# Performance work log

Hardware: AMD Instinct MI355X
Metric: run time of the kernel (lower is better)

The kernel has to match this reference:

```python
import jax, jax.numpy as jnp
import numpy as np

INPUT_SIZE = 128
HIDDEN_SIZE = 1024
OMEGA_IN = 0.5
OMEGA_B = 0.1
RHO = 0.9
L, N = 2048, 32


def setup_inputs() -> dict:
    key = jax.random.key(0)
    k_in, k_b, k_h, k_x = jax.random.split(key, 4)
    x = jax.random.normal(k_x, (L, N, INPUT_SIZE), dtype=jnp.float32)
    h_init = jnp.zeros((N, HIDDEN_SIZE), dtype=jnp.float32)
    W_in = jax.random.uniform(k_in, (HIDDEN_SIZE, INPUT_SIZE), minval=-OMEGA_IN, maxval=OMEGA_IN, dtype=jnp.float32)
    bias = jax.random.uniform(k_b, (HIDDEN_SIZE,), minval=-OMEGA_B, maxval=OMEGA_B, dtype=jnp.float32)
    # recurrent matrix rescaled to spectral radius RHO (as in the torch __init__)
    W_h_np = np.asarray(jax.random.uniform(k_h, (HIDDEN_SIZE, HIDDEN_SIZE), minval=-1.0, maxval=1.0, dtype=jnp.float32))
    sr = np.abs(np.linalg.eigvals(W_h_np)).max()
    W_h = jnp.asarray((W_h_np / sr * RHO).astype(np.float32))
    return {"input": x, "h_init": h_init, "W_in": W_in, "bias": bias, "W_h": W_h}


def reference(input, h_init, W_in, bias, W_h):
    # Pre-compute input projection for all timesteps in one GEMM: (L,N,H)
    x_proj = jnp.einsum('lni,hi->lnh', input, W_in) + bias

    def step(h, xp_t):
        h = jnp.tanh(xp_t + h @ W_h.T)
        return h, h

    _, states = jax.lax.scan(step, h_init, x_proj)
    return states  # (L, N, H)
```

## Files before the change

### kernel.cpp

```cpp
#include <hip/hip_runtime.h>
#include <stdint.h>

#define LSTEPS 2048
#define NB 32
#define IS 128
#define HS 1024
#define NGROUPS 8
#define WPG 32
#define BPG 4
#define CPW 32
#define NTHREADS 256
#define FLAG_SLOTS 8


__global__ __launch_bounds__(NTHREADS, 1)
void reservoir_scan(const float* __restrict__ x,
                    const float* __restrict__ h_init,
                    const float* __restrict__ W_in,
                    const float* __restrict__ bias,
                    const float* __restrict__ W_h,
                    float* __restrict__ out,
                    unsigned int* __restrict__ flags) {
  const int b    = blockIdx.x;
  const int g    = b & 7;
  const int wg   = b >> 3;
  const int tid  = threadIdx.x;
  const int w    = tid >> 6;
  const int lane = tid & 63;
  const int jbase = wg * CPW;
  const int nbase = g * BPG;

  __shared__ __align__(16) float wh_lds[CPW * HS];
  __shared__ __align__(16) float h_lds[BPG * HS];
  __shared__ __align__(16) float x_lds[BPG * IS];

  for (int e = tid * 4; e < CPW * HS; e += NTHREADS * 4)
    *(float4*)&wh_lds[e] = *(const float4*)&W_h[(size_t)jbase * HS + e];

  float2 wireg[8];
  #pragma unroll
  for (int jj = 0; jj < 8; ++jj)
    wireg[jj] = *(const float2*)&W_in[(size_t)(jbase + w * 8 + jj) * IS + lane * 2];

  const int onn = (lane & 31) >> 3;
  const int ojj = lane & 7;
  const float my_bias = bias[jbase + w * 8 + ojj];

  #pragma unroll 1
  for (int t = 0; t < LSTEPS; ++t) {
    {
      const float* xsrc = x + (size_t)(t * NB + nbase) * IS;
      for (int e = tid; e < BPG * IS; e += NTHREADS)
        x_lds[e] = xsrc[e];
    }

    if (t > 0) {
      const unsigned int target = (unsigned int)t;
      const unsigned int* fl =
          flags + (((size_t)(g * FLAG_SLOTS + ((t - 1) & (FLAG_SLOTS - 1))) * WPG + wg) << 5);
      int tries = 0;
      for (;;) {
        unsigned int v = (lane < WPG)
            ? __hip_atomic_load(&fl[lane], __ATOMIC_RELAXED, __HIP_MEMORY_SCOPE_AGENT)
            : target;
        if (__all(v == target)) break;
        if (++tries > 3) __builtin_amdgcn_s_sleep(1);
      }
      const float* hsrc = out + (size_t)((t - 1) * NB + nbase) * HS;
      float hv[16];
      #pragma unroll
      for (int i = 0; i < 16; ++i) {
        const int ii = (i + wg) & 15;
        hv[i] = __hip_atomic_load(&hsrc[tid + ii * NTHREADS], __ATOMIC_RELAXED,
                                  __HIP_MEMORY_SCOPE_AGENT);
      }
      #pragma unroll
      for (int i = 0; i < 16; ++i) {
        const int ii = (i + wg) & 15;
        h_lds[tid + ii * NTHREADS] = hv[i];
      }
    } else {
      const float* hsrc = h_init + (size_t)nbase * HS;
      #pragma unroll
      for (int i = 0; i < 16; ++i)
        h_lds[tid + i * NTHREADS] = hsrc[tid + i * NTHREADS];
    }
    __syncthreads();

    float acc[8][4];
    #pragma unroll
    for (int jj = 0; jj < 8; ++jj)
      #pragma unroll
      for (int nn = 0; nn < 4; ++nn) acc[jj][nn] = 0.f;

    {
      float2 xv[4];
      #pragma unroll
      for (int nn = 0; nn < 4; ++nn)
        xv[nn] = *(const float2*)&x_lds[nn * IS + lane * 2];
      #pragma unroll
      for (int jj = 0; jj < 8; ++jj) {
        const float2 wv = wireg[jj];
        #pragma unroll
        for (int nn = 0; nn < 4; ++nn)
          acc[jj][nn] += wv.x * xv[nn].x + wv.y * xv[nn].y;
      }
    }

    #pragma unroll
    for (int u = 0; u < 4; ++u) {
      const int k = u * 256 + lane * 4;
      float4 hv4[4];
      #pragma unroll
      for (int nn = 0; nn < 4; ++nn)
        hv4[nn] = *(const float4*)&h_lds[nn * HS + k];
      #pragma unroll
      for (int jj = 0; jj < 8; ++jj) {
        const float4 wv = *(const float4*)&wh_lds[(w * 8 + jj) * HS + k];
        #pragma unroll
        for (int nn = 0; nn < 4; ++nn) {
          acc[jj][nn] += wv.x * hv4[nn].x;
          acc[jj][nn] += wv.y * hv4[nn].y;
          acc[jj][nn] += wv.z * hv4[nn].z;
          acc[jj][nn] += wv.w * hv4[nn].w;
        }
      }
    }

    float a0[32];
    #pragma unroll
    for (int jj = 0; jj < 8; ++jj)
      #pragma unroll
      for (int nn = 0; nn < 4; ++nn)
        a0[nn * 8 + jj] = acc[jj][nn];

    float a1[16];
    {
      const int bit = lane & 1;
      #pragma unroll
      for (int q = 0; q < 16; ++q) {
        const float give = bit ? a0[2 * q] : a0[2 * q + 1];
        const float keep = bit ? a0[2 * q + 1] : a0[2 * q];
        a1[q] = keep + __shfl_xor(give, 1);
      }
    }
    float a2[8];
    {
      const int bit = (lane >> 1) & 1;
      #pragma unroll
      for (int q = 0; q < 8; ++q) {
        const float give = bit ? a1[2 * q] : a1[2 * q + 1];
        const float keep = bit ? a1[2 * q + 1] : a1[2 * q];
        a2[q] = keep + __shfl_xor(give, 2);
      }
    }
    float a3[4];
    {
      const int bit = (lane >> 2) & 1;
      #pragma unroll
      for (int q = 0; q < 4; ++q) {
        const float give = bit ? a2[2 * q] : a2[2 * q + 1];
        const float keep = bit ? a2[2 * q + 1] : a2[2 * q];
        a3[q] = keep + __shfl_xor(give, 4);
      }
    }
    float a4[2];
    {
      const int bit = (lane >> 3) & 1;
      #pragma unroll
      for (int q = 0; q < 2; ++q) {
        const float give = bit ? a3[2 * q] : a3[2 * q + 1];
        const float keep = bit ? a3[2 * q + 1] : a3[2 * q];
        a4[q] = keep + __shfl_xor(give, 8);
      }
    }
    float a5;
    {
      const int bit = (lane >> 4) & 1;
      const float give = bit ? a4[0] : a4[1];
      const float keep = bit ? a4[1] : a4[0];
      a5 = keep + __shfl_xor(give, 16);
    }
    const float r = a5 + __shfl_xor(a5, 32);

    if (lane < 32) {
      const float s = tanhf(r + my_bias);
      float* dst = out + (size_t)(t * NB + nbase + onn) * HS + (jbase + w * 8 + ojj);
      __hip_atomic_store(dst, s, __ATOMIC_RELAXED, __HIP_MEMORY_SCOPE_AGENT);
    }
    __syncthreads();

    if (tid < WPG) {
      unsigned int* fp =
          &flags[(((size_t)(g * FLAG_SLOTS + (t & (FLAG_SLOTS - 1))) * WPG + tid) << 5) + wg];
      __hip_atomic_store(fp, (unsigned int)(t + 1), __ATOMIC_RELEASE,
                         __HIP_MEMORY_SCOPE_AGENT);
    }
  }
}

extern "C" void kernel_launch(void* const* d_in, const int* in_sizes, int n_in,
                              void* d_out, int out_size, void* d_ws, size_t ws_size,
                              hipStream_t stream) {
  const float* x     = (const float*)d_in[0];
  const float* h0    = (const float*)d_in[1];
  const float* W_in  = (const float*)d_in[2];
  const float* bias  = (const float*)d_in[3];
  const float* W_h   = (const float*)d_in[4];
  float* out = (float*)d_out;
  unsigned int* flags = (unsigned int*)d_ws;

  hipLaunchKernelGGL(reservoir_scan, dim3(NGROUPS * WPG), dim3(NTHREADS), 0, stream,
                     x, h0, W_in, bias, W_h, out, flags);
}
```

Baseline: 11.52 ms.

## Load hidden state directly into registers per wave, drop LDS staging and barrier

Each wave now reads the previous hidden state and the input slice straight from global memory into registers. This replaces the block-cooperative copy into LDS and the __syncthreads that followed it, removing one barrier and an LDS round trip from the serial per-step critical path. In exchange every one of the four waves loads the full 4x1024 hidden slice itself, which is four times the global/L2 traffic, using scalar atomic loads. The change also adds a spin-wait timeout and a memset of the flag buffer before launch.

```diff
diff --git a/kernel.cpp b/kernel.cpp
--- a/kernel.cpp
+++ b/kernel.cpp
@@ -11,6 +11,7 @@
 #define CPW 32
 #define NTHREADS 256
 #define FLAG_SLOTS 8
+#define FLAG_BYTES (NGROUPS * FLAG_SLOTS * WPG * 32 * 4)
 
 
 __global__ __launch_bounds__(NTHREADS, 1)
@@ -31,8 +32,6 @@
   const int nbase = g * BPG;
 
   __shared__ __align__(16) float wh_lds[CPW * HS];
-  __shared__ __align__(16) float h_lds[BPG * HS];
-  __shared__ __align__(16) float x_lds[BPG * IS];
 
   for (int e = tid * 4; e < CPW * HS; e += NTHREADS * 4)
     *(float4*)&wh_lds[e] = *(const float4*)&W_h[(size_t)jbase * HS + e];
@@ -46,12 +45,16 @@
   const int ojj = lane & 7;
   const float my_bias = bias[jbase + w * 8 + ojj];
 
+  __syncthreads();
+
   #pragma unroll 1
   for (int t = 0; t < LSTEPS; ++t) {
+    float2 xv[4];
     {
       const float* xsrc = x + (size_t)(t * NB + nbase) * IS;
-      for (int e = tid; e < BPG * IS; e += NTHREADS)
-        x_lds[e] = xsrc[e];
+      #pragma unroll
+      for (int nn = 0; nn < 4; ++nn)
+        xv[nn] = *(const float2*)&xsrc[nn * IS + lane * 2];
     }
 
     if (t > 0) {
@@ -64,28 +67,23 @@
             ? __hip_atomic_load(&fl[lane], __ATOMIC_RELAXED, __HIP_MEMORY_SCOPE_AGENT)
             : target;
         if (__all(v == target)) break;
-        if (++tries > 3) __builtin_amdgcn_s_sleep(1);
-      }
-      const float* hsrc = out + (size_t)((t - 1) * NB + nbase) * HS;
-      float hv[16];
-      #pragma unroll
-      for (int i = 0; i < 16; ++i) {
-        const int ii = (i + wg) & 15;
-        hv[i] = __hip_atomic_load(&hsrc[tid + ii * NTHREADS], __ATOMIC_RELAXED,
-                                  __HIP_MEMORY_SCOPE_AGENT);
-      }
-      #pragma unroll
-      for (int i = 0; i < 16; ++i) {
-        const int ii = (i + wg) & 15;
-        h_lds[tid + ii * NTHREADS] = hv[i];
-      }
-    } else {
-      const float* hsrc = h_init + (size_t)nbase * HS;
-      #pragma unroll
-      for (int i = 0; i < 16; ++i)
-        h_lds[tid + i * NTHREADS] = hsrc[tid + i * NTHREADS];
-    }
-    __syncthreads();
+        if (++tries > (1 << 18)) break;
+        if (tries > 3) __builtin_amdgcn_s_sleep(1);
+      }
+    }
+    asm volatile("" ::: "memory");
+
+    const float* hsrc = (t > 0) ? out + (size_t)((t - 1) * NB + nbase) * HS
+                                : h_init + (size_t)nbase * HS;
+    float hx[4][4][4];
+    #pragma unroll
+    for (int u = 0; u < 4; ++u)
+      #pragma unroll
+      for (int nn = 0; nn < 4; ++nn)
+        #pragma unroll
+        for (int c = 0; c < 4; ++c)
+          hx[u][nn][c] = __hip_atomic_load(&hsrc[(size_t)nn * HS + u * 256 + lane * 4 + c],
+                                           __ATOMIC_RELAXED, __HIP_MEMORY_SCOPE_AGENT);
 
     float acc[8][4];
     #pragma unroll
@@ -93,36 +91,26 @@
       #pragma unroll
       for (int nn = 0; nn < 4; ++nn) acc[jj][nn] = 0.f;
 
-    {
-      float2 xv[4];
-      #pragma unroll
-      for (int nn = 0; nn < 4; ++nn)
-        xv[nn] = *(const float2*)&x_lds[nn * IS + lane * 2];
-      #pragma unroll
-      for (int jj = 0; jj < 8; ++jj) {
-        const float2 wv = wireg[jj];
-        #pragma unroll
-        for (int nn = 0; nn < 4; ++nn)
-          acc[jj][nn] += wv.x * xv[nn].x + wv.y * xv[nn].y;
-      }
+    #pragma unroll
+    for (int jj = 0; jj < 8; ++jj) {
+      const float2 wv = wireg[jj];
+      #pragma unroll
+      for (int nn = 0; nn < 4; ++nn)
+        acc[jj][nn] += wv.x * xv[nn].x + wv.y * xv[nn].y;
     }
 
     #pragma unroll
     for (int u = 0; u < 4; ++u) {
       const int k = u * 256 + lane * 4;
-      float4 hv4[4];
-      #pragma unroll
-      for (int nn = 0; nn < 4; ++nn)
-        hv4[nn] = *(const float4*)&h_lds[nn * HS + k];
       #pragma unroll
       for (int jj = 0; jj < 8; ++jj) {
         const float4 wv = *(const float4*)&wh_lds[(w * 8 + jj) * HS + k];
         #pragma unroll
         for (int nn = 0; nn < 4; ++nn) {
-          acc[jj][nn] += wv.x * hv4[nn].x;
-          acc[jj][nn] += wv.y * hv4[nn].y;
-          acc[jj][nn] += wv.z * hv4[nn].z;
-          acc[jj][nn] += wv.w * hv4[nn].w;
+          acc[jj][nn] += wv.x * hx[u][nn][0];
+          acc[jj][nn] += wv.y * hx[u][nn][1];
+          acc[jj][nn] += wv.z * hx[u][nn][2];
+          acc[jj][nn] += wv.w * hx[u][nn][3];
         }
       }
     }
@@ -210,6 +198,8 @@
   float* out = (float*)d_out;
   unsigned int* flags = (unsigned int*)d_ws;
 
+  hipMemsetAsync(flags, 0, FLAG_BYTES, stream);
+
   hipLaunchKernelGGL(reservoir_scan, dim3(NGROUPS * WPG), dim3(NTHREADS), 0, stream,
                      x, h0, W_in, bias, W_h, out, flags);
 }
```

Result: slower. 17.48 ms (+51.8%).
